# Kernel optimization log

Hardware: AMD Instinct MI355X
Metric: run time of the kernel (lower is better)

Reference implementation:

```python
import jax, jax.numpy as jnp
import numpy as np

ROT_DIM = 32
THETA = 10000.0
HEAD_SIZE = 192


def _rope(t):
    # t: [B, T, D]; rotate first ROT_DIM features with interleaved-pair RoPE
    T = t.shape[1]
    inv_freq = 1.0 / (THETA ** (jnp.arange(0, ROT_DIM, 2, dtype=jnp.float32) / ROT_DIM))  # [16]
    freqs = jnp.arange(T, dtype=jnp.float32)[:, None] * inv_freq[None, :]  # [T,16]
    freqs = jnp.repeat(freqs, 2, axis=-1)  # [T,32], each freq repeated for the pair
    cos = jnp.cos(freqs).astype(t.dtype)
    sin = jnp.sin(freqs).astype(t.dtype)
    x = t[..., :ROT_DIM]
    x1 = x[..., 0::2]
    x2 = x[..., 1::2]
    rot_half = jnp.stack([-x2, x1], axis=-1).reshape(x.shape)  # interleave (-x2, x1)
    rotated = x * cos + rot_half * sin
    return jnp.concatenate([rotated, t[..., ROT_DIM:]], axis=-1)


def setup_inputs() -> dict:
    key = jax.random.key(0)
    k1, k2, k3, k4 = jax.random.split(key, 4)
    B, T, C, H = 64, 512, 768, HEAD_SIZE
    x = jax.random.normal(k1, (B, T, C), dtype=jnp.float32)
    s = 1.0 / np.sqrt(C)
    Wq = jax.random.normal(k2, (C, H), dtype=jnp.float32) * s
    Wk = jax.random.normal(k3, (C, H), dtype=jnp.float32) * s
    Wv = jax.random.normal(k4, (C, H), dtype=jnp.float32) * s
    return {"x": x, "Wq": Wq, "Wk": Wk, "Wv": Wv}


def reference(x, Wq, Wk, Wv):
    B, T, C = x.shape
    q = x @ Wq  # [B,T,H]
    k = x @ Wk
    v = x @ Wv
    q = _rope(q)
    k = _rope(k)
    scale = k.shape[-1] ** -0.5
    scores = jnp.einsum('bqh,bkh->bqk', q, k) * scale  # [B,T,T]
    causal = jnp.tril(jnp.ones((T, T), dtype=bool))
    scores = jnp.where(causal[None, :, :], scores, -jnp.inf)
    weight = jax.nn.softmax(scores, axis=-1)
    # dropout is identity at eval time
    out = jnp.einsum('bqk,bkh->bqh', weight, v)  # [B,T,H]
    return out
```

## Files before the change

### kernel.cpp

```cpp
#include <hip/hip_runtime.h>
#include <cstdint>

typedef __attribute__((ext_vector_type(8))) short short8;
typedef __attribute__((ext_vector_type(4))) float floatx4;

__device__ __forceinline__ unsigned short f2bf(float f) {
  uint32_t u = __builtin_bit_cast(uint32_t, f);
  u += 0x7fffu + ((u >> 16) & 1u);
  return (unsigned short)(u >> 16);
}
__device__ __forceinline__ uint32_t pkbf(float lo, float hi) {
  uint32_t a = __builtin_bit_cast(uint32_t, lo) + 0x8000u;
  uint32_t b = __builtin_bit_cast(uint32_t, hi) + 0x8000u;
  return __builtin_amdgcn_perm(b, a, 0x07060302);
}

__global__ void prep_w_kernel(const float* __restrict__ Wq,
                              const float* __restrict__ Wk,
                              const float* __restrict__ Wv,
                              unsigned short* __restrict__ Wt) {
  int idx = blockIdx.x * 256 + threadIdx.x;
  if (idx >= 576 * 768) return;
  int n = idx / 768;
  int k = idx - n * 768;
  int which = n / 192;
  int nn = n - which * 192;
  const float* W = (which == 0) ? Wq : (which == 1) ? Wk : Wv;
  Wt[idx] = f2bf(W[k * 192 + nn]);
}

__global__ __launch_bounds__(256) void proj_kernel(
    const float* __restrict__ x, const unsigned short* __restrict__ Wt_all,
    unsigned short* __restrict__ q_ws, unsigned short* __restrict__ k_ws,
    unsigned short* __restrict__ v_ws) {
  __shared__ __align__(16) unsigned short A_lds[64 * 40];
  __shared__ __align__(16) unsigned short B_lds[192 * 40];
  const int tid = threadIdx.x;
  const int w = tid >> 6, l = tid & 63, quad = l >> 4, ln = l & 15;
  const int m0 = blockIdx.x * 64;
  const int which = blockIdx.y;
  const unsigned short* Wt = Wt_all + which * 192 * 768;

  const int arow = tid >> 3, ac4 = tid & 7;
  const int brow = tid >> 2, bc = tid & 3;

  floatx4 acc[12];
#pragma unroll
  for (int nt = 0; nt < 12; ++nt) acc[nt] = floatx4{0.f, 0.f, 0.f, 0.f};

  for (int kb = 0; kb < 24; ++kb) {
    const int k0 = kb * 32;
#pragma unroll
    for (int it = 0; it < 2; ++it) {
      float4 f = *(const float4*)(x + (size_t)(m0 + arow + it * 32) * 768 + k0 + ac4 * 4);
      uint2 p = {pkbf(f.x, f.y), pkbf(f.z, f.w)};
      *(uint2*)&A_lds[(arow + it * 32) * 40 + ac4 * 4] = p;
    }
#pragma unroll
    for (int it = 0; it < 3; ++it) {
      uint4 v = *(const uint4*)(Wt + (brow + it * 64) * 768 + k0 + bc * 8);
      *(uint4*)&B_lds[(brow + it * 64) * 40 + bc * 8] = v;
    }
    __syncthreads();
    short8 a0 = *(const short8*)&A_lds[(w * 16 + ln) * 40 + quad * 8];
#pragma unroll
    for (int nt = 0; nt < 12; ++nt) {
      short8 bfr = *(const short8*)&B_lds[(nt * 16 + ln) * 40 + quad * 8];
      acc[nt] = __builtin_amdgcn_mfma_f32_16x16x32_bf16(a0, bfr, acc[nt], 0, 0, 0);
    }
    __syncthreads();
  }

  if (which == 2) {
    int rb = m0 + w * 16 + quad * 4;
    int bb = rb >> 9, t = rb & 511;
#pragma unroll
    for (int nt = 0; nt < 12; ++nt) {
      ushort4 pv;
      pv.x = f2bf(acc[nt][0]); pv.y = f2bf(acc[nt][1]);
      pv.z = f2bf(acc[nt][2]); pv.w = f2bf(acc[nt][3]);
      *(ushort4*)&v_ws[((size_t)bb * 192 + nt * 16 + ln) * 512 + t] = pv;
    }
  } else {
    unsigned short* dst = (which == 0) ? q_ws : k_ws;
#pragma unroll
    for (int r = 0; r < 4; ++r) {
      int row_g = m0 + w * 16 + quad * 4 + r;
      int t_pos = row_g & 511;
      float vals[12];
#pragma unroll
      for (int nt = 0; nt < 12; ++nt) vals[nt] = acc[nt][r];
#pragma unroll
      for (int nt = 0; nt < 2; ++nt) {
        int col = nt * 16 + ln;
        float v = vals[nt];
        float pv = __shfl_xor(v, 1);
        int i = col >> 1;
        float inv_freq = exp2f(-(float)i * (13.287712379549449f / 16.0f));
        float ang = (float)t_pos * inv_freq;
        float sv, cv;
        sincosf(ang, &sv, &cv);
        vals[nt] = (col & 1) ? (v * cv + pv * sv) : (v * cv - pv * sv);
      }
#pragma unroll
      for (int nt = 0; nt < 12; ++nt)
        dst[row_g * 192 + nt * 16 + ln] = f2bf(vals[nt]);
    }
  }
}

__global__ __launch_bounds__(256) void attn_kernel(
    const unsigned short* __restrict__ q_ws, const unsigned short* __restrict__ k_ws,
    const unsigned short* __restrict__ v_ws, float* __restrict__ out) {
  __shared__ __align__(16) unsigned short K_lds[64 * 200];
  __shared__ __align__(16) unsigned short V_lds[192 * 72];
  __shared__ __align__(16) unsigned short P_lds[4][16 * 72];
  const int tid = threadIdx.x;
  const int w = tid >> 6, l = tid & 63, quad = l >> 4, ln = l & 15;
  const int b = blockIdx.y;
  const int qt = (blockIdx.y < 32) ? blockIdx.x : 7 - blockIdx.x;
  const int q0 = qt * 64;

  short8 qf[6];
  {
    const unsigned short* qp =
        q_ws + (size_t)(b * 512 + q0 + w * 16 + ln) * 192 + quad * 8;
#pragma unroll
    for (int kk = 0; kk < 6; ++kk) qf[kk] = *(const short8*)(qp + kk * 32);
  }

  float m_i[4], l_i[4];
  floatx4 o[12];
#pragma unroll
  for (int r = 0; r < 4; ++r) { m_i[r] = -1e30f; l_i[r] = 0.f; }
#pragma unroll
  for (int nt = 0; nt < 12; ++nt) o[nt] = floatx4{0.f, 0.f, 0.f, 0.f};
  const float sm_scale = 0.07216878364870323f;

  for (int kt = 0; kt <= qt; ++kt) {
    const int k0 = kt * 64;
    __syncthreads();
#pragma unroll
    for (int it = 0; it < 6; ++it) {
      int idx = it * 256 + tid;
      int row = idx / 24, c = idx - row * 24;
      uint4 v = *(const uint4*)(k_ws + (size_t)(b * 512 + k0 + row) * 192 + c * 8);
      *(uint4*)&K_lds[row * 200 + c * 8] = v;
    }
#pragma unroll
    for (int it = 0; it < 6; ++it) {
      int idx = it * 256 + tid;
      int row = idx >> 3, c = idx & 7;
      uint4 v = *(const uint4*)(v_ws + (size_t)(b * 192 + row) * 512 + k0 + c * 8);
      *(uint4*)&V_lds[row * 72 + c * 8] = v;
    }
    __syncthreads();

    float s[4][4];
#pragma unroll
    for (int nt = 0; nt < 4; ++nt) {
      floatx4 sa = floatx4{0.f, 0.f, 0.f, 0.f};
#pragma unroll
      for (int kk = 0; kk < 6; ++kk) {
        short8 kf = *(const short8*)&K_lds[(nt * 16 + ln) * 200 + kk * 32 + quad * 8];
        sa = __builtin_amdgcn_mfma_f32_16x16x32_bf16(qf[kk], kf, sa, 0, 0, 0);
      }
#pragma unroll
      for (int r = 0; r < 4; ++r) s[nt][r] = sa[r] * sm_scale;
    }
    if (kt == qt) {
#pragma unroll
      for (int nt = 0; nt < 4; ++nt)
#pragma unroll
        for (int r = 0; r < 4; ++r)
          if (nt * 16 + ln > w * 16 + quad * 4 + r) s[nt][r] = -1e30f;
    }
    float alpha[4];
#pragma unroll
    for (int r = 0; r < 4; ++r) {
      float mx = fmaxf(fmaxf(s[0][r], s[1][r]), fmaxf(s[2][r], s[3][r]));
      mx = fmaxf(mx, __shfl_xor(mx, 1));
      mx = fmaxf(mx, __shfl_xor(mx, 2));
      mx = fmaxf(mx, __shfl_xor(mx, 4));
      mx = fmaxf(mx, __shfl_xor(mx, 8));
      float mnew = fmaxf(m_i[r], mx);
      alpha[r] = __expf(m_i[r] - mnew);
      float sum = 0.f;
#pragma unroll
      for (int nt = 0; nt < 4; ++nt) {
        s[nt][r] = __expf(s[nt][r] - mnew);
        sum += s[nt][r];
      }
      sum += __shfl_xor(sum, 1);
      sum += __shfl_xor(sum, 2);
      sum += __shfl_xor(sum, 4);
      sum += __shfl_xor(sum, 8);
      l_i[r] = l_i[r] * alpha[r] + sum;
      m_i[r] = mnew;
    }
#pragma unroll
    for (int nt = 0; nt < 12; ++nt)
#pragma unroll
      for (int r = 0; r < 4; ++r) o[nt][r] *= alpha[r];

#pragma unroll
    for (int nt = 0; nt < 4; ++nt)
#pragma unroll
      for (int r = 0; r < 4; ++r)
        P_lds[w][(quad * 4 + r) * 72 + nt * 16 + ln] = f2bf(s[nt][r]);
    __asm__ volatile("s_waitcnt lgkmcnt(0)" ::: "memory");

#pragma unroll
    for (int ks = 0; ks < 2; ++ks) {
      short8 pf = *(const short8*)&P_lds[w][ln * 72 + ks * 32 + quad * 8];
#pragma unroll
      for (int nt = 0; nt < 12; ++nt) {
        short8 vf = *(const short8*)&V_lds[(nt * 16 + ln) * 72 + ks * 32 + quad * 8];
        o[nt] = __builtin_amdgcn_mfma_f32_16x16x32_bf16(pf, vf, o[nt], 0, 0, 0);
      }
    }
  }

#pragma unroll
  for (int r = 0; r < 4; ++r) {
    float inv = 1.0f / l_i[r];
    size_t rowoff = (size_t)(b * 512 + q0 + w * 16 + quad * 4 + r) * 192;
#pragma unroll
    for (int nt = 0; nt < 12; ++nt)
      out[rowoff + nt * 16 + ln] = o[nt][r] * inv;
  }
}

extern "C" void kernel_launch(void* const* d_in, const int* in_sizes, int n_in,
                              void* d_out, int out_size, void* d_ws, size_t ws_size,
                              hipStream_t stream) {
  const float* x = (const float*)d_in[0];
  const float* Wq = (const float*)d_in[1];
  const float* Wk = (const float*)d_in[2];
  const float* Wv = (const float*)d_in[3];
  float* out = (float*)d_out;

  char* ws = (char*)d_ws;
  const size_t QKV_BYTES = (size_t)64 * 512 * 192 * 2;
  unsigned short* q_ws = (unsigned short*)(ws);
  unsigned short* k_ws = (unsigned short*)(ws + QKV_BYTES);
  unsigned short* v_ws = (unsigned short*)(ws + 2 * QKV_BYTES);
  unsigned short* Wt = (unsigned short*)(ws + 3 * QKV_BYTES);

  hipLaunchKernelGGL(prep_w_kernel, dim3(1728), dim3(256), 0, stream, Wq, Wk, Wv, Wt);
  hipLaunchKernelGGL(proj_kernel, dim3(512, 3), dim3(256), 0, stream, x, Wt, q_ws, k_ws, v_ws);
  hipLaunchKernelGGL(attn_kernel, dim3(8, 64), dim3(256), 0, stream, q_ws, k_ws, v_ws, out);
}
```

Baseline: 239.5 us.

## Fuse QKV projection into one block tile and prefetch K/V in attention

The projection kernel now computes all 576 Q/K/V output columns per 64-row block, so x is read and converted once instead of three times. It uses a swizzled unpadded LDS layout, a 2x2 warp tiling with 2x18 MFMA tiles per warp, and register double-buffering of the global loads. The attention kernel prefetches the next K/V tile into registers while computing on the current one and raises wave priority around the MFMA sections. Both kernels add launch bounds for two blocks per CU. The cost is much higher register pressure: the 72 accumulators per thread in the projection plus the prefetch buffers could cause spills or lower occupancy.

```diff
diff --git a/kernel.cpp b/kernel.cpp
--- a/kernel.cpp
+++ b/kernel.cpp
@@ -29,87 +29,158 @@
   Wt[idx] = f2bf(W[k * 192 + nn]);
 }
 
-__global__ __launch_bounds__(256) void proj_kernel(
-    const float* __restrict__ x, const unsigned short* __restrict__ Wt_all,
+__global__ __launch_bounds__(256, 2) void proj_kernel(
+    const float* __restrict__ x, const unsigned short* __restrict__ Wt,
     unsigned short* __restrict__ q_ws, unsigned short* __restrict__ k_ws,
     unsigned short* __restrict__ v_ws) {
-  __shared__ __align__(16) unsigned short A_lds[64 * 40];
-  __shared__ __align__(16) unsigned short B_lds[192 * 40];
+  __shared__ __align__(16) unsigned short A_lds[64 * 32];
+  __shared__ __align__(16) unsigned short B_lds[576 * 32];
   const int tid = threadIdx.x;
   const int w = tid >> 6, l = tid & 63, quad = l >> 4, ln = l & 15;
+  const int wr = w & 1, wc = w >> 1;
   const int m0 = blockIdx.x * 64;
-  const int which = blockIdx.y;
-  const unsigned short* Wt = Wt_all + which * 192 * 768;
-
-  const int arow = tid >> 3, ac4 = tid & 7;
-  const int brow = tid >> 2, bc = tid & 3;
-
-  floatx4 acc[12];
-#pragma unroll
-  for (int nt = 0; nt < 12; ++nt) acc[nt] = floatx4{0.f, 0.f, 0.f, 0.f};
-
-  for (int kb = 0; kb < 24; ++kb) {
-    const int k0 = kb * 32;
-#pragma unroll
-    for (int it = 0; it < 2; ++it) {
-      float4 f = *(const float4*)(x + (size_t)(m0 + arow + it * 32) * 768 + k0 + ac4 * 4);
-      uint2 p = {pkbf(f.x, f.y), pkbf(f.z, f.w)};
-      *(uint2*)&A_lds[(arow + it * 32) * 40 + ac4 * 4] = p;
-    }
-#pragma unroll
-    for (int it = 0; it < 3; ++it) {
-      uint4 v = *(const uint4*)(Wt + (brow + it * 64) * 768 + k0 + bc * 8);
-      *(uint4*)&B_lds[(brow + it * 64) * 40 + bc * 8] = v;
-    }
-    __syncthreads();
-    short8 a0 = *(const short8*)&A_lds[(w * 16 + ln) * 40 + quad * 8];
-#pragma unroll
-    for (int nt = 0; nt < 12; ++nt) {
-      short8 bfr = *(const short8*)&B_lds[(nt * 16 + ln) * 40 + quad * 8];
-      acc[nt] = __builtin_amdgcn_mfma_f32_16x16x32_bf16(a0, bfr, acc[nt], 0, 0, 0);
-    }
-    __syncthreads();
-  }
-
-  if (which == 2) {
-    int rb = m0 + w * 16 + quad * 4;
-    int bb = rb >> 9, t = rb & 511;
-#pragma unroll
-    for (int nt = 0; nt < 12; ++nt) {
-      ushort4 pv;
-      pv.x = f2bf(acc[nt][0]); pv.y = f2bf(acc[nt][1]);
-      pv.z = f2bf(acc[nt][2]); pv.w = f2bf(acc[nt][3]);
-      *(ushort4*)&v_ws[((size_t)bb * 192 + nt * 16 + ln) * 512 + t] = pv;
+
+  const int arow = tid >> 2;
+  const int ac = tid & 3;
+  const int aslot = ((ac ^ ((tid >> 3) & 3)) << 4);
+  char* Awp = (char*)A_lds + arow * 64 + aslot;
+  char* Bwp = (char*)B_lds + arow * 64 + aslot;
+
+  const float* xp = x + (size_t)(m0 + arow) * 768 + ac * 8;
+  const unsigned short* bp = Wt + (size_t)arow * 768 + ac * 8;
+
+  const int fq = ((quad ^ ((ln >> 1) & 3)) << 4);
+  const char* Arp = (const char*)A_lds + (wr * 32 + ln) * 64 + fq;
+  const char* Brp = (const char*)B_lds + (wc * 288 + ln) * 64 + fq;
+
+  floatx4 acc[2][18];
+#pragma unroll
+  for (int mi = 0; mi < 2; ++mi)
+#pragma unroll
+    for (int nj = 0; nj < 18; ++nj) acc[mi][nj] = floatx4{0.f, 0.f, 0.f, 0.f};
+
+  float4 a0x, a0y, a1x, a1y;
+  uint4 bb0[9], bb1[9];
+
+#define LOADA(AX, AY, K0)                    \
+  do {                                       \
+    AX = *(const float4*)(xp + (K0));        \
+    AY = *(const float4*)(xp + (K0) + 4);    \
+  } while (0)
+#define LOADB(BB, K0)                                             \
+  do {                                                            \
+    _Pragma("unroll") for (int it = 0; it < 9; ++it)              \
+        (BB)[it] = *(const uint4*)(bp + it * 49152 + (K0));       \
+  } while (0)
+#define STAGE(AX, AY, BB)                                         \
+  do {                                                            \
+    uint4 ap;                                                     \
+    ap.x = pkbf((AX).x, (AX).y);                                  \
+    ap.y = pkbf((AX).z, (AX).w);                                  \
+    ap.z = pkbf((AY).x, (AY).y);                                  \
+    ap.w = pkbf((AY).z, (AY).w);                                  \
+    *(uint4*)Awp = ap;                                            \
+    _Pragma("unroll") for (int it = 0; it < 9; ++it)              \
+        *(uint4*)(Bwp + it * 4096) = (BB)[it];                    \
+  } while (0)
+#define PCOMPUTE()                                                               \
+  do {                                                                           \
+    short8 af0 = *(const short8*)(Arp);                                          \
+    short8 af1 = *(const short8*)(Arp + 1024);                                   \
+    _Pragma("unroll") for (int nj = 0; nj < 18; ++nj) {                          \
+      short8 bf = *(const short8*)(Brp + nj * 1024);                             \
+      acc[0][nj] = __builtin_amdgcn_mfma_f32_16x16x32_bf16(af0, bf, acc[0][nj],  \
+                                                           0, 0, 0);             \
+      acc[1][nj] = __builtin_amdgcn_mfma_f32_16x16x32_bf16(af1, bf, acc[1][nj],  \
+                                                           0, 0, 0);             \
+    }                                                                            \
+  } while (0)
+
+  LOADA(a0x, a0y, 0);
+  LOADB(bb0, 0);
+  for (int kb = 0; kb < 24; kb += 2) {
+    LOADA(a1x, a1y, (kb + 1) * 32);
+    STAGE(a0x, a0y, bb0);
+    __syncthreads();
+    LOADB(bb1, (kb + 1) * 32);
+    PCOMPUTE();
+    __syncthreads();
+    if (kb < 22) LOADA(a0x, a0y, (kb + 2) * 32);
+    STAGE(a1x, a1y, bb1);
+    __syncthreads();
+    if (kb < 22) LOADB(bb0, (kb + 2) * 32);
+    PCOMPUTE();
+    __syncthreads();
+  }
+#undef LOADA
+#undef LOADB
+#undef STAGE
+#undef PCOMPUTE
+
+  if (wc == 0) {
+#pragma unroll
+    for (int mi = 0; mi < 2; ++mi) {
+#pragma unroll
+      for (int r = 0; r < 4; ++r) {
+        int row_g = m0 + wr * 32 + mi * 16 + quad * 4 + r;
+        int t_pos = row_g & 511;
+        float vq[2], vk[2];
+#pragma unroll
+        for (int tt = 0; tt < 2; ++tt) {
+          vq[tt] = acc[mi][tt][r];
+          vk[tt] = acc[mi][12 + tt][r];
+        }
+#pragma unroll
+        for (int tt = 0; tt < 2; ++tt) {
+          int col = tt * 16 + ln;
+          int i = col >> 1;
+          float inv_freq = exp2f(-(float)i * (13.287712379549449f / 16.0f));
+          float ang = (float)t_pos * inv_freq;
+          float sv, cv;
+          sincosf(ang, &sv, &cv);
+          float pq = __shfl_xor(vq[tt], 1);
+          float pk = __shfl_xor(vk[tt], 1);
+          vq[tt] = (col & 1) ? (vq[tt] * cv + pq * sv) : (vq[tt] * cv - pq * sv);
+          vk[tt] = (col & 1) ? (vk[tt] * cv + pk * sv) : (vk[tt] * cv - pk * sv);
+        }
+#pragma unroll
+        for (int nj = 0; nj < 12; ++nj) {
+          float v = (nj < 2) ? vq[nj] : acc[mi][nj][r];
+          q_ws[(size_t)row_g * 192 + nj * 16 + ln] = f2bf(v);
+        }
+#pragma unroll
+        for (int nj = 0; nj < 6; ++nj) {
+          float v = (nj < 2) ? vk[nj] : acc[mi][12 + nj][r];
+          k_ws[(size_t)row_g * 192 + nj * 16 + ln] = f2bf(v);
+        }
+      }
     }
   } else {
-    unsigned short* dst = (which == 0) ? q_ws : k_ws;
-#pragma unroll
-    for (int r = 0; r < 4; ++r) {
-      int row_g = m0 + w * 16 + quad * 4 + r;
-      int t_pos = row_g & 511;
-      float vals[12];
-#pragma unroll
-      for (int nt = 0; nt < 12; ++nt) vals[nt] = acc[nt][r];
-#pragma unroll
-      for (int nt = 0; nt < 2; ++nt) {
-        int col = nt * 16 + ln;
-        float v = vals[nt];
-        float pv = __shfl_xor(v, 1);
-        int i = col >> 1;
-        float inv_freq = exp2f(-(float)i * (13.287712379549449f / 16.0f));
-        float ang = (float)t_pos * inv_freq;
-        float sv, cv;
-        sincosf(ang, &sv, &cv);
-        vals[nt] = (col & 1) ? (v * cv + pv * sv) : (v * cv - pv * sv);
-      }
-#pragma unroll
-      for (int nt = 0; nt < 12; ++nt)
-        dst[row_g * 192 + nt * 16 + ln] = f2bf(vals[nt]);
-    }
-  }
-}
-
-__global__ __launch_bounds__(256) void attn_kernel(
+#pragma unroll
+    for (int mi = 0; mi < 2; ++mi) {
+#pragma unroll
+      for (int r = 0; r < 4; ++r) {
+        int row_g = m0 + wr * 32 + mi * 16 + quad * 4 + r;
+#pragma unroll
+        for (int nj = 0; nj < 6; ++nj)
+          k_ws[(size_t)row_g * 192 + 96 + nj * 16 + ln] = f2bf(acc[mi][nj][r]);
+      }
+      int rb = m0 + wr * 32 + mi * 16 + quad * 4;
+      int bb = rb >> 9, t = rb & 511;
+#pragma unroll
+      for (int nj = 6; nj < 18; ++nj) {
+        ushort4 pv;
+        pv.x = f2bf(acc[mi][nj][0]);
+        pv.y = f2bf(acc[mi][nj][1]);
+        pv.z = f2bf(acc[mi][nj][2]);
+        pv.w = f2bf(acc[mi][nj][3]);
+        *(ushort4*)&v_ws[((size_t)bb * 192 + (nj - 6) * 16 + ln) * 512 + t] = pv;
+      }
+    }
+  }
+}
+
+__global__ __launch_bounds__(256, 2) void attn_kernel(
     const unsigned short* __restrict__ q_ws, const unsigned short* __restrict__ k_ws,
     const unsigned short* __restrict__ v_ws, float* __restrict__ out) {
   __shared__ __align__(16) unsigned short K_lds[64 * 200];
@@ -137,26 +208,44 @@
   for (int nt = 0; nt < 12; ++nt) o[nt] = floatx4{0.f, 0.f, 0.f, 0.f};
   const float sm_scale = 0.07216878364870323f;
 
+  uint4 kpre0[6], vpre0[6], kpre1[6], vpre1[6];
+
+#define AT_LOAD(KB, VB, K0)                                                        \
+  do {                                                                             \
+    _Pragma("unroll") for (int it = 0; it < 6; ++it) {                             \
+      int idx = it * 256 + tid;                                                    \
+      int row = idx / 24, c = idx - row * 24;                                      \
+      (KB)[it] = *(const uint4*)(k_ws + (size_t)(b * 512 + (K0) + row) * 192 + c * 8); \
+    }                                                                              \
+    _Pragma("unroll") for (int it = 0; it < 6; ++it) {                             \
+      int idx = it * 256 + tid;                                                    \
+      int row = idx >> 3, c = idx & 7;                                             \
+      (VB)[it] = *(const uint4*)(v_ws + (size_t)(b * 192 + row) * 512 + (K0) + c * 8); \
+    }                                                                              \
+  } while (0)
+#define AT_STAGE(KB, VB)                                      \
+  do {                                                        \
+    _Pragma("unroll") for (int it = 0; it < 6; ++it) {        \
+      int idx = it * 256 + tid;                               \
+      int row = idx / 24, c = idx - row * 24;                 \
+      *(uint4*)&K_lds[row * 200 + c * 8] = (KB)[it];          \
+    }                                                         \
+    _Pragma("unroll") for (int it = 0; it < 6; ++it) {        \
+      int idx = it * 256 + tid;                               \
+      int row = idx >> 3, c = idx & 7;                        \
+      *(uint4*)&V_lds[row * 72 + c * 8] = (VB)[it];           \
+    }                                                         \
+  } while (0)
+
+  AT_LOAD(kpre0, vpre0, 0);
+
   for (int kt = 0; kt <= qt; ++kt) {
-    const int k0 = kt * 64;
-    __syncthreads();
-#pragma unroll
-    for (int it = 0; it < 6; ++it) {
-      int idx = it * 256 + tid;
-      int row = idx / 24, c = idx - row * 24;
-      uint4 v = *(const uint4*)(k_ws + (size_t)(b * 512 + k0 + row) * 192 + c * 8);
-      *(uint4*)&K_lds[row * 200 + c * 8] = v;
-    }
-#pragma unroll
-    for (int it = 0; it < 6; ++it) {
-      int idx = it * 256 + tid;
-      int row = idx >> 3, c = idx & 7;
-      uint4 v = *(const uint4*)(v_ws + (size_t)(b * 192 + row) * 512 + k0 + c * 8);
-      *(uint4*)&V_lds[row * 72 + c * 8] = v;
-    }
-    __syncthreads();
+    AT_STAGE(kpre0, vpre0);
+    __syncthreads();
+    if (kt < qt) AT_LOAD(kpre1, vpre1, (kt + 1) * 64);
 
     float s[4][4];
+    __builtin_amdgcn_s_setprio(1);
 #pragma unroll
     for (int nt = 0; nt < 4; ++nt) {
       floatx4 sa = floatx4{0.f, 0.f, 0.f, 0.f};
@@ -168,6 +257,7 @@
 #pragma unroll
       for (int r = 0; r < 4; ++r) s[nt][r] = sa[r] * sm_scale;
     }
+    __builtin_amdgcn_s_setprio(0);
     if (kt == qt) {
 #pragma unroll
       for (int nt = 0; nt < 4; ++nt)
@@ -210,6 +300,7 @@
         P_lds[w][(quad * 4 + r) * 72 + nt * 16 + ln] = f2bf(s[nt][r]);
     __asm__ volatile("s_waitcnt lgkmcnt(0)" ::: "memory");
 
+    __builtin_amdgcn_s_setprio(1);
 #pragma unroll
     for (int ks = 0; ks < 2; ++ks) {
       short8 pf = *(const short8*)&P_lds[w][ln * 72 + ks * 32 + quad * 8];
@@ -219,7 +310,18 @@
         o[nt] = __builtin_amdgcn_mfma_f32_16x16x32_bf16(pf, vf, o[nt], 0, 0, 0);
       }
     }
-  }
+    __builtin_amdgcn_s_setprio(0);
+    __syncthreads();
+    if (kt < qt) {
+#pragma unroll
+      for (int it = 0; it < 6; ++it) {
+        kpre0[it] = kpre1[it];
+        vpre0[it] = vpre1[it];
+      }
+    }
+  }
+#undef AT_LOAD
+#undef AT_STAGE
 
 #pragma unroll
   for (int r = 0; r < 4; ++r) {
@@ -248,6 +350,6 @@
   unsigned short* Wt = (unsigned short*)(ws + 3 * QKV_BYTES);
 
   hipLaunchKernelGGL(prep_w_kernel, dim3(1728), dim3(256), 0, stream, Wq, Wk, Wv, Wt);
-  hipLaunchKernelGGL(proj_kernel, dim3(512, 3), dim3(256), 0, stream, x, Wt, q_ws, k_ws, v_ws);
+  hipLaunchKernelGGL(proj_kernel, dim3(512), dim3(256), 0, stream, x, Wt, q_ws, k_ws, v_ws);
   hipLaunchKernelGGL(attn_kernel, dim3(8, 64), dim3(256), 0, stream, q_ws, k_ws, v_ws, out);
 }
```

After: 438.7 us. 83.1% more time.

## Restructure QKV projection with double-buffered async LDS loads and wider tiles

Applied to the files above, without the earlier changes.

The projection kernel is reworked. Each block now computes 288 output columns across a 2x2 wave grid, so the fp32 x tile is read and converted twice instead of three times. The prep kernel writes weights in a pre-swizzled, k-blocked bf16 image so they can be copied straight into double-buffered LDS with global_load_lds, overlapping the next tile's loads with MFMA work. The epilogue is split by role to route the column ranges to q, k and v with RoPE applied. The attention kernel also raises wave priority around its MFMA sections, at the cost of more complex index logic and higher register pressure.

```diff
diff --git a/kernel.cpp b/kernel.cpp
--- a/kernel.cpp
+++ b/kernel.cpp
@@ -14,99 +14,209 @@
   uint32_t b = __builtin_bit_cast(uint32_t, hi) + 0x8000u;
   return __builtin_amdgcn_perm(b, a, 0x07060302);
 }
+__device__ __forceinline__ void gll16(const void* g, void* l) {
+  __builtin_amdgcn_global_load_lds(
+      (const __attribute__((address_space(1))) unsigned int*)g,
+      (__attribute__((address_space(3))) unsigned int*)l, 16, 0, 0);
+}
 
 __global__ void prep_w_kernel(const float* __restrict__ Wq,
                               const float* __restrict__ Wk,
                               const float* __restrict__ Wv,
                               unsigned short* __restrict__ Wt) {
-  int idx = blockIdx.x * 256 + threadIdx.x;
-  if (idx >= 576 * 768) return;
-  int n = idx / 768;
-  int k = idx - n * 768;
-  int which = n / 192;
-  int nn = n - which * 192;
+  int id = blockIdx.x * 256 + threadIdx.x;
+  int by = id / 27648, rem = id - by * 27648;
+  int kb = rem / 1152, s = rem - kb * 1152;
+  int row = s >> 2, cs = s & 3;
+  int n = by * 288 + row;
+  int c = cs ^ ((row >> 1) & 3);
+  int which = n / 192, nn = n - which * 192;
   const float* W = (which == 0) ? Wq : (which == 1) ? Wk : Wv;
-  Wt[idx] = f2bf(W[k * 192 + nn]);
-}
-
-__global__ __launch_bounds__(256) void proj_kernel(
-    const float* __restrict__ x, const unsigned short* __restrict__ Wt_all,
+  int k0 = kb * 32 + c * 8;
+  unsigned short v[8];
+#pragma unroll
+  for (int e = 0; e < 8; ++e) v[e] = f2bf(W[(size_t)(k0 + e) * 192 + nn]);
+  uint4 o;
+  o.x = v[0] | ((uint32_t)v[1] << 16);
+  o.y = v[2] | ((uint32_t)v[3] << 16);
+  o.z = v[4] | ((uint32_t)v[5] << 16);
+  o.w = v[6] | ((uint32_t)v[7] << 16);
+  *(uint4*)(Wt + (size_t)id * 8) = o;
+}
+
+__global__ __launch_bounds__(256, 3) void proj_kernel(
+    const float* __restrict__ x, const unsigned short* __restrict__ Wt,
     unsigned short* __restrict__ q_ws, unsigned short* __restrict__ k_ws,
     unsigned short* __restrict__ v_ws) {
-  __shared__ __align__(16) unsigned short A_lds[64 * 40];
-  __shared__ __align__(16) unsigned short B_lds[192 * 40];
+  __shared__ __align__(16) unsigned short A_lds[2][64 * 32];
+  __shared__ __align__(16) unsigned short B_lds[2][288 * 32];
   const int tid = threadIdx.x;
   const int w = tid >> 6, l = tid & 63, quad = l >> 4, ln = l & 15;
+  const int wr = w & 1, wc = w >> 1;
   const int m0 = blockIdx.x * 64;
-  const int which = blockIdx.y;
-  const unsigned short* Wt = Wt_all + which * 192 * 768;
-
-  const int arow = tid >> 3, ac4 = tid & 7;
-  const int brow = tid >> 2, bc = tid & 3;
-
-  floatx4 acc[12];
-#pragma unroll
-  for (int nt = 0; nt < 12; ++nt) acc[nt] = floatx4{0.f, 0.f, 0.f, 0.f};
-
+
+  const int arow = tid >> 2, ac = tid & 3;
+  const int aslot = ((ac ^ ((arow >> 1) & 3)) << 4);
+  const float* xp = x + (size_t)(m0 + arow) * 768 + ac * 8;
+  const unsigned short* wimg = Wt + (size_t)blockIdx.y * 27648 * 8;
+
+  const int fq = ((quad ^ ((ln >> 1) & 3)) << 4);
+
+  floatx4 acc[2][9];
+#pragma unroll
+  for (int mi = 0; mi < 2; ++mi)
+#pragma unroll
+    for (int nj = 0; nj < 9; ++nj) acc[mi][nj] = floatx4{0.f, 0.f, 0.f, 0.f};
+
+  float4 a0x, a0y;
+
+#define LOADA(K0)                                  \
+  do {                                             \
+    a0x = *(const float4*)(xp + (K0));             \
+    a0y = *(const float4*)(xp + (K0) + 4);         \
+  } while (0)
+#define STAGEA(BUF)                                               \
+  do {                                                            \
+    uint4 ap;                                                     \
+    ap.x = pkbf(a0x.x, a0x.y);                                    \
+    ap.y = pkbf(a0x.z, a0x.w);                                    \
+    ap.z = pkbf(a0y.x, a0y.y);                                    \
+    ap.w = pkbf(a0y.z, a0y.w);                                    \
+    *(uint4*)((char*)&A_lds[BUF][0] + arow * 64 + aslot) = ap;    \
+  } while (0)
+#define LOADB(KB, BUF)                                               \
+  do {                                                               \
+    const unsigned short* src = wimg + (size_t)(KB) * 9216;          \
+    char* dstb = (char*)&B_lds[BUF][0];                              \
+    _Pragma("unroll") for (int it = 0; it < 4; ++it)                 \
+        gll16(src + (it * 256 + tid) * 8, dstb + (it * 256 + tid) * 16); \
+    if (tid < 128) gll16(src + (1024 + tid) * 8, dstb + (1024 + tid) * 16); \
+  } while (0)
+#define PCOMPUTE(BUF)                                                            \
+  do {                                                                           \
+    short8 af0 = *(const short8*)((const char*)&A_lds[BUF][0] +                  \
+                                  (wr * 32 + ln) * 64 + fq);                     \
+    short8 af1 = *(const short8*)((const char*)&A_lds[BUF][0] +                  \
+                                  (wr * 32 + 16 + ln) * 64 + fq);                \
+    _Pragma("unroll") for (int nj = 0; nj < 9; ++nj) {                           \
+      short8 bf = *(const short8*)((const char*)&B_lds[BUF][0] +                 \
+                                   (wc * 144 + nj * 16 + ln) * 64 + fq);         \
+      acc[0][nj] = __builtin_amdgcn_mfma_f32_16x16x32_bf16(af0, bf, acc[0][nj],  \
+                                                           0, 0, 0);             \
+      acc[1][nj] = __builtin_amdgcn_mfma_f32_16x16x32_bf16(af1, bf, acc[1][nj],  \
+                                                           0, 0, 0);             \
+    }                                                                            \
+  } while (0)
+
+  LOADB(0, 0);
+  LOADA(0);
+  STAGEA(0);
+  LOADA(32);
+  __syncthreads();
+
+#pragma unroll 2
   for (int kb = 0; kb < 24; ++kb) {
-    const int k0 = kb * 32;
-#pragma unroll
-    for (int it = 0; it < 2; ++it) {
-      float4 f = *(const float4*)(x + (size_t)(m0 + arow + it * 32) * 768 + k0 + ac4 * 4);
-      uint2 p = {pkbf(f.x, f.y), pkbf(f.z, f.w)};
-      *(uint2*)&A_lds[(arow + it * 32) * 40 + ac4 * 4] = p;
-    }
-#pragma unroll
-    for (int it = 0; it < 3; ++it) {
-      uint4 v = *(const uint4*)(Wt + (brow + it * 64) * 768 + k0 + bc * 8);
-      *(uint4*)&B_lds[(brow + it * 64) * 40 + bc * 8] = v;
-    }
+    const int cur = kb & 1, nxt = cur ^ 1;
+    if (kb < 23) {
+      LOADB(kb + 1, nxt);
+      STAGEA(nxt);
+    }
+    if (kb < 22) LOADA((kb + 2) * 32);
+    PCOMPUTE(cur);
     __syncthreads();
-    short8 a0 = *(const short8*)&A_lds[(w * 16 + ln) * 40 + quad * 8];
-#pragma unroll
-    for (int nt = 0; nt < 12; ++nt) {
-      short8 bfr = *(const short8*)&B_lds[(nt * 16 + ln) * 40 + quad * 8];
-      acc[nt] = __builtin_amdgcn_mfma_f32_16x16x32_bf16(a0, bfr, acc[nt], 0, 0, 0);
-    }
-    __syncthreads();
-  }
-
-  if (which == 2) {
-    int rb = m0 + w * 16 + quad * 4;
-    int bb = rb >> 9, t = rb & 511;
-#pragma unroll
-    for (int nt = 0; nt < 12; ++nt) {
-      ushort4 pv;
-      pv.x = f2bf(acc[nt][0]); pv.y = f2bf(acc[nt][1]);
-      pv.z = f2bf(acc[nt][2]); pv.w = f2bf(acc[nt][3]);
-      *(ushort4*)&v_ws[((size_t)bb * 192 + nt * 16 + ln) * 512 + t] = pv;
+  }
+#undef LOADA
+#undef STAGEA
+#undef LOADB
+#undef PCOMPUTE
+
+  const float R_LG = 0.8304820237218406f;
+#define ROPE2(V0, V1, TPOS)                                         \
+  do {                                                              \
+    float i0 = (float)(ln >> 1);                                    \
+    float f0 = exp2f(-i0 * R_LG);                                   \
+    float f1 = exp2f(-(i0 + 8.0f) * R_LG);                          \
+    float s0, c0, s1, c1;                                           \
+    sincosf((float)(TPOS)*f0, &s0, &c0);                            \
+    sincosf((float)(TPOS)*f1, &s1, &c1);                            \
+    float p0 = __shfl_xor(V0, 1), p1 = __shfl_xor(V1, 1);           \
+    V0 = (ln & 1) ? (V0 * c0 + p0 * s0) : (V0 * c0 - p0 * s0);      \
+    V1 = (ln & 1) ? (V1 * c1 + p1 * s1) : (V1 * c1 - p1 * s1);      \
+  } while (0)
+
+  const int role = blockIdx.y * 2 + wc;
+  if (role == 0) {
+#pragma unroll
+    for (int mi = 0; mi < 2; ++mi)
+#pragma unroll
+      for (int r = 0; r < 4; ++r) {
+        int row_g = m0 + wr * 32 + mi * 16 + quad * 4 + r;
+        int t_pos = row_g & 511;
+        float v0 = acc[mi][0][r], v1 = acc[mi][1][r];
+        ROPE2(v0, v1, t_pos);
+        q_ws[(size_t)row_g * 192 + ln] = f2bf(v0);
+        q_ws[(size_t)row_g * 192 + 16 + ln] = f2bf(v1);
+#pragma unroll
+        for (int nj = 2; nj < 9; ++nj)
+          q_ws[(size_t)row_g * 192 + nj * 16 + ln] = f2bf(acc[mi][nj][r]);
+      }
+  } else if (role == 1) {
+#pragma unroll
+    for (int mi = 0; mi < 2; ++mi)
+#pragma unroll
+      for (int r = 0; r < 4; ++r) {
+        int row_g = m0 + wr * 32 + mi * 16 + quad * 4 + r;
+        int t_pos = row_g & 511;
+        float v0 = acc[mi][3][r], v1 = acc[mi][4][r];
+        ROPE2(v0, v1, t_pos);
+#pragma unroll
+        for (int nj = 0; nj < 3; ++nj)
+          q_ws[(size_t)row_g * 192 + 144 + nj * 16 + ln] = f2bf(acc[mi][nj][r]);
+        k_ws[(size_t)row_g * 192 + ln] = f2bf(v0);
+        k_ws[(size_t)row_g * 192 + 16 + ln] = f2bf(v1);
+#pragma unroll
+        for (int nj = 5; nj < 9; ++nj)
+          k_ws[(size_t)row_g * 192 + (nj - 3) * 16 + ln] = f2bf(acc[mi][nj][r]);
+      }
+  } else if (role == 2) {
+#pragma unroll
+    for (int mi = 0; mi < 2; ++mi) {
+#pragma unroll
+      for (int r = 0; r < 4; ++r) {
+        int row_g = m0 + wr * 32 + mi * 16 + quad * 4 + r;
+#pragma unroll
+        for (int nj = 0; nj < 6; ++nj)
+          k_ws[(size_t)row_g * 192 + 96 + nj * 16 + ln] = f2bf(acc[mi][nj][r]);
+      }
+      int rb = m0 + wr * 32 + mi * 16 + quad * 4;
+      int bb = rb >> 9, t = rb & 511;
+#pragma unroll
+      for (int nj = 6; nj < 9; ++nj) {
+        ushort4 pv;
+        pv.x = f2bf(acc[mi][nj][0]);
+        pv.y = f2bf(acc[mi][nj][1]);
+        pv.z = f2bf(acc[mi][nj][2]);
+        pv.w = f2bf(acc[mi][nj][3]);
+        *(ushort4*)&v_ws[((size_t)bb * 192 + (nj - 6) * 16 + ln) * 512 + t] = pv;
+      }
     }
   } else {
-    unsigned short* dst = (which == 0) ? q_ws : k_ws;
-#pragma unroll
-    for (int r = 0; r < 4; ++r) {
-      int row_g = m0 + w * 16 + quad * 4 + r;
-      int t_pos = row_g & 511;
-      float vals[12];
-#pragma unroll
-      for (int nt = 0; nt < 12; ++nt) vals[nt] = acc[nt][r];
-#pragma unroll
-      for (int nt = 0; nt < 2; ++nt) {
-        int col = nt * 16 + ln;
-        float v = vals[nt];
-        float pv = __shfl_xor(v, 1);
-        int i = col >> 1;
-        float inv_freq = exp2f(-(float)i * (13.287712379549449f / 16.0f));
-        float ang = (float)t_pos * inv_freq;
-        float sv, cv;
-        sincosf(ang, &sv, &cv);
-        vals[nt] = (col & 1) ? (v * cv + pv * sv) : (v * cv - pv * sv);
-      }
-#pragma unroll
-      for (int nt = 0; nt < 12; ++nt)
-        dst[row_g * 192 + nt * 16 + ln] = f2bf(vals[nt]);
-    }
-  }
+#pragma unroll
+    for (int mi = 0; mi < 2; ++mi) {
+      int rb = m0 + wr * 32 + mi * 16 + quad * 4;
+      int bb = rb >> 9, t = rb & 511;
+#pragma unroll
+      for (int nj = 0; nj < 9; ++nj) {
+        ushort4 pv;
+        pv.x = f2bf(acc[mi][nj][0]);
+        pv.y = f2bf(acc[mi][nj][1]);
+        pv.z = f2bf(acc[mi][nj][2]);
+        pv.w = f2bf(acc[mi][nj][3]);
+        *(ushort4*)&v_ws[((size_t)bb * 192 + 48 + nj * 16 + ln) * 512 + t] = pv;
+      }
+    }
+  }
+#undef ROPE2
 }
 
 __global__ __launch_bounds__(256) void attn_kernel(
@@ -157,6 +267,7 @@
     __syncthreads();
 
     float s[4][4];
+    __builtin_amdgcn_s_setprio(1);
 #pragma unroll
     for (int nt = 0; nt < 4; ++nt) {
       floatx4 sa = floatx4{0.f, 0.f, 0.f, 0.f};
@@ -168,6 +279,7 @@
 #pragma unroll
       for (int r = 0; r < 4; ++r) s[nt][r] = sa[r] * sm_scale;
     }
+    __builtin_amdgcn_s_setprio(0);
     if (kt == qt) {
 #pragma unroll
       for (int nt = 0; nt < 4; ++nt)
@@ -210,6 +322,7 @@
         P_lds[w][(quad * 4 + r) * 72 + nt * 16 + ln] = f2bf(s[nt][r]);
     __asm__ volatile("s_waitcnt lgkmcnt(0)" ::: "memory");
 
+    __builtin_amdgcn_s_setprio(1);
 #pragma unroll
     for (int ks = 0; ks < 2; ++ks) {
       short8 pf = *(const short8*)&P_lds[w][ln * 72 + ks * 32 + quad * 8];
@@ -219,6 +332,7 @@
         o[nt] = __builtin_amdgcn_mfma_f32_16x16x32_bf16(pf, vf, o[nt], 0, 0, 0);
       }
     }
+    __builtin_amdgcn_s_setprio(0);
   }
 
 #pragma unroll
@@ -247,7 +361,7 @@
   unsigned short* v_ws = (unsigned short*)(ws + 2 * QKV_BYTES);
   unsigned short* Wt = (unsigned short*)(ws + 3 * QKV_BYTES);
 
-  hipLaunchKernelGGL(prep_w_kernel, dim3(1728), dim3(256), 0, stream, Wq, Wk, Wv, Wt);
-  hipLaunchKernelGGL(proj_kernel, dim3(512, 3), dim3(256), 0, stream, x, Wt, q_ws, k_ws, v_ws);
+  hipLaunchKernelGGL(prep_w_kernel, dim3(216), dim3(256), 0, stream, Wq, Wk, Wv, Wt);
+  hipLaunchKernelGGL(proj_kernel, dim3(512, 2), dim3(256), 0, stream, x, Wt, q_ws, k_ws, v_ws);
   hipLaunchKernelGGL(attn_kernel, dim3(8, 64), dim3(256), 0, stream, q_ws, k_ws, v_ws, out);
 }
```

Result: faster. 229.4 us (-4.3%).
